# Optimization experiments

Measured on AMD Instinct MI355X. Metric: run time of the kernel, lower is better.

Reference implementation:

```python
import jax, jax.numpy as jnp
import numpy as np

S, NL = 64, 5000          # num_sequences, num_labels
PD, LD = 1024, 768        # protein / label embedding dims
DIM, OD = 512, 512        # latent_dim, output_dim


def setup_inputs() -> dict:
    key = jax.random.key(0)
    ks = jax.random.split(key, 8)
    sc = lambda f: 1.0 / np.sqrt(f).astype(np.float32)
    return {
        "P_f": jax.random.normal(ks[0], (S, PD), jnp.float32),
        "label_emb": jax.random.normal(ks[1], (NL, LD), jnp.float32),
        "W_p": jax.random.normal(ks[2], (DIM, PD), jnp.float32) * sc(PD),
        "W_l": jax.random.normal(ks[3], (DIM, LD), jnp.float32) * sc(LD),
        "W1": jax.random.normal(ks[4], (OD, 2 * DIM), jnp.float32) * sc(2 * DIM),
        "b1": jnp.zeros((OD,), jnp.float32),
        "W2": jax.random.normal(ks[5], (OD, OD), jnp.float32) * sc(OD),
        "b2": jnp.zeros((OD,), jnp.float32),
        "W3": jax.random.normal(ks[6], (1, OD), jnp.float32) * sc(OD),
        "b3": jnp.zeros((1,), jnp.float32),
        "L": jnp.arange(NL, dtype=jnp.int64),
    }


def reference(P_f, label_emb, W_p, W_l, W1, b1, W2, b2, W3, b3, L):
    # label lookup (cached_label_embeddings(L)) + linear projections
    L_f = label_emb[L]                      # [NL, LD]
    P_e = P_f @ W_p.T                       # [S, DIM]
    L_e = L_f @ W_l.T                       # [NL, DIM]
    # joint cat([P_e_expanded, L_e_expanded]) @ W1.T  ==  P-side + L-side GEMMs,
    # broadcast-summed (avoids materializing the [S*NL, 2*DIM] concat)
    hp = P_e @ W1[:, :DIM].T                # [S, OD]
    hl = L_e @ W1[:, DIM:].T                # [NL, OD]
    h = jax.nn.relu(hp[:, None, :] + hl[None, :, :] + b1)   # [S, NL, OD]
    h = jax.nn.relu(jnp.einsum("snd,od->sno", h, W2) + b2)  # [S, NL, OD]
    logits = jnp.einsum("sno,o->sn", h, W3[0]) + b3[0]      # [S, NL]
    return logits
```

## Files before the change

kernel.cpp:

```cpp
#include <hip/hip_runtime.h>
#include <hip/hip_bf16.h>

typedef short short8 __attribute__((ext_vector_type(8)));
typedef float f32x4 __attribute__((ext_vector_type(4)));

#define S_   64
#define NL_  5000
#define PD_  1024
#define LD_  768
#define DIM_ 512
#define OD_  512

#define BK     32
#define NWIN4  4
#define KSTEPS 16
#define NT_M   79
#define HL_RT  157

__device__ __forceinline__ ushort f2bf(float f) {
    union { float f; unsigned u; } v; v.f = f;
    unsigned r = v.u + 0x7fffu + ((v.u >> 16) & 1u);
    return (ushort)(r >> 16);
}
__device__ __forceinline__ float bf2f(ushort h) {
    union { unsigned u; float f; } v; v.u = ((unsigned)h) << 16;
    return v.f;
}
__device__ __forceinline__ int swz(int row, int kslot) {
    return (row * 64 + kslot * 16) ^ (((row >> 1) & 7) << 4);
}

__device__ __forceinline__ void proj8(
    float* Af , const float* __restrict__ A, int lda, int K,
    const float* __restrict__ W, int ldw, const float* __restrict__ bias,
    float* __restrict__ C, int o0, int t) {
    const int s = t & 63, og = t >> 6;
    const int oA = o0 + og * 2, oB = oA + 1;
    float acc0 = 0.f, acc1 = 0.f;
    for (int ck = 0; ck < K; ck += 256) {
        __syncthreads();
#pragma unroll
        for (int it = 0; it < 16; it++) {
            int r = it * 4 + (t >> 6);
            float4 v = *(const float4*)(A + (size_t)r * lda + ck + (t & 63) * 4);
            *(float4*)(Af + r * 258 + (t & 63) * 4) = v;
        }
        __syncthreads();
        const float* w0 = W + (size_t)oA * ldw + ck;
        const float* w1 = W + (size_t)oB * ldw + ck;
        const float* ar = Af + s * 258;
#pragma unroll 8
        for (int k4 = 0; k4 < 64; k4++) {
            f32x4 a4 = *(const f32x4*)(ar + k4 * 4);
            float4 v0 = *(const float4*)(w0 + k4 * 4);
            float4 v1 = *(const float4*)(w1 + k4 * 4);
            acc0 += a4[0] * v0.x + a4[1] * v0.y + a4[2] * v0.z + a4[3] * v0.w;
            acc1 += a4[0] * v1.x + a4[1] * v1.y + a4[2] * v1.z + a4[3] * v1.w;
        }
    }
    C[s * DIM_ + oA] = acc0 + (bias ? bias[oA] : 0.f);
    C[s * DIM_ + oB] = acc1 + (bias ? bias[oB] : 0.f);
}

__global__ __launch_bounds__(256) void k_pre1(
    const float* __restrict__ W2, const float* __restrict__ W_l,
    const float* __restrict__ W1, const float* __restrict__ P_f,
    const float* __restrict__ W_p,
    char* __restrict__ panel, ushort* __restrict__ MlT, float* __restrict__ P_e) {
    __shared__ float lbuf[64 * 258];
    int b = blockIdx.x, t = threadIdx.x;
    if (b < 128) {
        int c = b * 256 + t;
        int o = c >> 6, rem = c & 63, kt = rem >> 2, kslot = rem & 3;
        const float* src = W2 + o * DIM_ + kt * BK + kslot * 8;
        float4 v0 = *(const float4*)src;
        float4 v1 = *(const float4*)(src + 4);
        union { ushort u[8]; short8 v; } pk;
        pk.u[0] = f2bf(v0.x); pk.u[1] = f2bf(v0.y); pk.u[2] = f2bf(v0.z); pk.u[3] = f2bf(v0.w);
        pk.u[4] = f2bf(v1.x); pk.u[5] = f2bf(v1.y); pk.u[6] = f2bf(v1.z); pk.u[7] = f2bf(v1.w);
        *(short8*)(panel + kt * 32768 + (o >> 4) * 1024 + kslot * 256 + (o & 15) * 16) = pk.v;
    } else if (b < 320) {
        float (*w1r)[DIM_] = (float (*)[DIM_])lbuf;
        int bx = b - 128;
        int o0 = (bx / 3) * 8;
        int ld = (bx % 3) * 256 + t;
        for (int i = t; i < 8 * DIM_; i += 256)
            w1r[i >> 9][i & 511] = W1[(o0 + (i >> 9)) * (2 * DIM_) + DIM_ + (i & 511)];
        __syncthreads();
        float acc[8] = {};
        for (int dim = 0; dim < DIM_; dim += 4) {
            float wl0 = W_l[(dim + 0) * LD_ + ld];
            float wl1 = W_l[(dim + 1) * LD_ + ld];
            float wl2 = W_l[(dim + 2) * LD_ + ld];
            float wl3 = W_l[(dim + 3) * LD_ + ld];
#pragma unroll
            for (int oi = 0; oi < 8; oi++) {
                f32x4 wv = *(const f32x4*)&w1r[oi][dim];
                acc[oi] += wv[0] * wl0 + wv[1] * wl1 + wv[2] * wl2 + wv[3] * wl3;
            }
        }
#pragma unroll
        for (int oi = 0; oi < 8; oi++) MlT[(o0 + oi) * LD_ + ld] = f2bf(acc[oi]);
    } else {
        proj8(lbuf, P_f, PD_, PD_, W_p, PD_, nullptr, P_e, (b - 320) * 8, t);
    }
}

__global__ __launch_bounds__(256) void k_pre2(
    const float* __restrict__ P_e, const float* __restrict__ W1,
    const float* __restrict__ b1, const float* __restrict__ emb,
    const int* __restrict__ L, const ushort* __restrict__ MlT,
    float* __restrict__ hpb, ushort* __restrict__ hlB) {
    __shared__ float lbuf[64 * 258];
    int b = blockIdx.x, t = threadIdx.x;
    if (b < 64) {
        proj8(lbuf, P_e, DIM_, DIM_, W1, 2 * DIM_, b1, hpb, b * 8, t);
    } else {
        int hb = b - 64;
        int rblk = hb % HL_RT, oh = hb / HL_RT;
        int r0 = rblk * 32;
        int w = t >> 6, l = t & 63, lg = l >> 4, ll = l & 15;
        const float* arow[2];
#pragma unroll
        for (int mt = 0; mt < 2; mt++) {
            int r = r0 + mt * 16 + ll;
            if (r >= NL_) r = NL_ - 1;
            arow[mt] = emb + (size_t)L[r] * LD_ + lg * 8;
        }
        f32x4 acc[2][4] = {};
        for (int k = 0; k < LD_; k += 32) {
            short8 a[2], bf[4];
#pragma unroll
            for (int mt = 0; mt < 2; mt++) {
                float4 v0 = *(const float4*)(arow[mt] + k);
                float4 v1 = *(const float4*)(arow[mt] + k + 4);
                union { ushort u[8]; short8 v; } pk;
                pk.u[0] = f2bf(v0.x); pk.u[1] = f2bf(v0.y);
                pk.u[2] = f2bf(v0.z); pk.u[3] = f2bf(v0.w);
                pk.u[4] = f2bf(v1.x); pk.u[5] = f2bf(v1.y);
                pk.u[6] = f2bf(v1.z); pk.u[7] = f2bf(v1.w);
                a[mt] = pk.v;
            }
#pragma unroll
            for (int ot = 0; ot < 4; ot++) {
                int o = oh * 256 + w * 64 + ot * 16 + ll;
                bf[ot] = *(const short8*)(MlT + o * LD_ + k + lg * 8);
            }
#pragma unroll
            for (int mt = 0; mt < 2; mt++)
#pragma unroll
                for (int ot = 0; ot < 4; ot++)
                    acc[mt][ot] = __builtin_amdgcn_mfma_f32_16x16x32_bf16(a[mt], bf[ot], acc[mt][ot], 0, 0, 0);
        }
#pragma unroll
        for (int mt = 0; mt < 2; mt++)
#pragma unroll
            for (int ot = 0; ot < 4; ot++)
#pragma unroll
                for (int reg = 0; reg < 4; reg++) {
                    int r = r0 + mt * 16 + lg * 4 + reg;
                    if (r < NL_)
                        hlB[(size_t)r * DIM_ + oh * 256 + w * 64 + ot * 16 + ll] = f2bf(acc[mt][ot][reg]);
                }
    }
}

__global__ __launch_bounds__(512, 2) void k_main2(
    const ushort* __restrict__ hlB, const float* __restrict__ hpb,
    const char* __restrict__ panel, const float* __restrict__ b2,
    const float* __restrict__ W3, const float* __restrict__ b3,
    float* __restrict__ out) {
    __shared__ f32x4 ldsv[4096];
    char* lds = (char*)ldsv;
    const int t = threadIdx.x;
    const int n0 = blockIdx.x * 64, s0 = blockIdx.y * 2;
    const int w = t >> 6, lane = t & 63, lg = lane >> 4, ll = lane & 15;
    const int wr = w >> 2, wc = w & 3;

    const int arow = t >> 2, akslot = t & 3;
    int an = n0 + (arow & 63); if (an >= NL_) an = NL_ - 1;
    const ushort* hlsrc = hlB + (size_t)an * DIM_ + akslot * 8;
    const float*  hpsrc = hpb + (s0 + (arow >> 6)) * DIM_ + akslot * 8;
    const int awz = swz(arow, akslot);

    const int abase = swz(wr * 64 + ll, lg);
    const char* bbase = panel + (wc * 8) * 1024 + lane * 16;

    f32x4 acc[4][8] = {};

    auto packSub = [&](int buf, int sub, short8 hv, f32x4 p0, f32x4 p1) {
        float x[8];
#pragma unroll
        for (int e = 0; e < 4; e++) {
            float a0 = bf2f((ushort)hv[e]) + p0[e];
            float a1 = bf2f((ushort)hv[4 + e]) + p1[e];
            x[e]     = a0 > 0.f ? a0 : 0.f;
            x[4 + e] = a1 > 0.f ? a1 : 0.f;
        }
        union { __hip_bfloat162 h2[4]; short8 v; } pk;
#pragma unroll
        for (int e = 0; e < 4; e++)
            pk.h2[e] = __float22bfloat162_rn(make_float2(x[2 * e], x[2 * e + 1]));
        *(short8*)(lds + buf * 32768 + sub * 8192 + awz) = pk.v;
    };

    {
#pragma unroll
        for (int i = 0; i < 4; i++) {
            short8 hv = *(const short8*)(hlsrc + i * BK);
            f32x4 p0 = *(const f32x4*)(hpsrc + i * BK);
            f32x4 p1 = *(const f32x4*)(hpsrc + i * BK + 4);
            packSub(0, i, hv, p0, p1);
        }
        asm volatile("s_waitcnt lgkmcnt(0)" ::: "memory");
        __builtin_amdgcn_s_barrier();
    }
    short8 bq0[4], bq1[4];
#pragma unroll
    for (int j = 0; j < 4; j++) bq0[j] = *(const short8*)(bbase + j * 1024);

    short8 hvA, hvB; f32x4 pA0, pA1, pB0, pB1;

    for (int win = 0; win < NWIN4; win++) {
        const char* A = lds + (win & 1) * 32768;
        const int nxt = (win & 1) ^ 1;
        const bool more = (win + 1 < NWIN4);
#pragma unroll
        for (int i = 0; i < 4; i++) {
            const int ks = 4 * win + i;
            const char* bks = bbase + ks * 32768;
            short8 a[4];
#pragma unroll
            for (int mt = 0; mt < 4; mt++)
                a[mt] = *(const short8*)(A + i * 8192 + abase + mt * 1024);
#pragma unroll
            for (int j = 0; j < 4; j++) bq1[j] = *(const short8*)(bks + 4096 + j * 1024);
            if (more) {
                if (i == 0) {
                    hvA = *(const short8*)(hlsrc + (ks + 4) * BK);
                    pA0 = *(const f32x4*)(hpsrc + (ks + 4) * BK);
                    pA1 = *(const f32x4*)(hpsrc + (ks + 4) * BK + 4);
                } else if (i == 1) {
                    packSub(nxt, 0, hvA, pA0, pA1);
                    hvB = *(const short8*)(hlsrc + (ks + 4) * BK);
                    pB0 = *(const f32x4*)(hpsrc + (ks + 4) * BK);
                    pB1 = *(const f32x4*)(hpsrc + (ks + 4) * BK + 4);
                } else if (i == 2) {
                    packSub(nxt, 1, hvB, pB0, pB1);
                    hvA = *(const short8*)(hlsrc + (ks + 4) * BK);
                    pA0 = *(const f32x4*)(hpsrc + (ks + 4) * BK);
                    pA1 = *(const f32x4*)(hpsrc + (ks + 4) * BK + 4);
                } else {
                    packSub(nxt, 2, hvA, pA0, pA1);
                    hvB = *(const short8*)(hlsrc + (ks + 4) * BK);
                    pB0 = *(const f32x4*)(hpsrc + (ks + 4) * BK);
                    pB1 = *(const f32x4*)(hpsrc + (ks + 4) * BK + 4);
                }
            }
            __builtin_amdgcn_s_setprio(1);
#pragma unroll
            for (int mt = 0; mt < 4; mt++)
#pragma unroll
                for (int j = 0; j < 4; j++)
                    acc[mt][j] = __builtin_amdgcn_mfma_f32_16x16x32_bf16(a[mt], bq0[j], acc[mt][j], 0, 0, 0);
            __builtin_amdgcn_s_setprio(0);
            if (!(win == NWIN4 - 1 && i == 3))
#pragma unroll
                for (int j = 0; j < 4; j++)
                    bq0[j] = *(const short8*)(bbase + (ks + 1) * 32768 + j * 1024);
            __builtin_amdgcn_s_setprio(1);
#pragma unroll
            for (int mt = 0; mt < 4; mt++)
#pragma unroll
                for (int j = 0; j < 4; j++)
                    acc[mt][4 + j] = __builtin_amdgcn_mfma_f32_16x16x32_bf16(a[mt], bq1[j], acc[mt][4 + j], 0, 0, 0);
            __builtin_amdgcn_s_setprio(0);
        }
        if (more) packSub(nxt, 3, hvB, pB0, pB1);
        asm volatile("s_waitcnt lgkmcnt(0)" ::: "memory");
        __builtin_amdgcn_s_barrier();
    }

    float* logit = (float*)lds;
    if (t < 128) logit[t] = 0.f;
    __syncthreads();
#pragma unroll
    for (int mt = 0; mt < 4; mt++) {
        float p4[4] = { 0.f, 0.f, 0.f, 0.f };
#pragma unroll
        for (int ot = 0; ot < 8; ot++) {
            int o = wc * 128 + ot * 16 + ll;
            float bb = b2[o], w3 = W3[o];
#pragma unroll
            for (int reg = 0; reg < 4; reg++) {
                float v = acc[mt][ot][reg] + bb;
                v = v > 0.f ? v : 0.f;
                p4[reg] += v * w3;
            }
        }
#pragma unroll
        for (int m = 1; m < 16; m <<= 1)
#pragma unroll
            for (int reg = 0; reg < 4; reg++) p4[reg] += __shfl_xor(p4[reg], m, 64);
        if (ll == 0)
#pragma unroll
            for (int reg = 0; reg < 4; reg++)
                atomicAdd(&logit[wr * 64 + mt * 16 + lg * 4 + reg], p4[reg]);
    }
    __syncthreads();
    if (t < 128) {
        int n = n0 + (t & 63);
        int s = s0 + (t >> 6);
        if (n < NL_) out[(size_t)s * NL_ + n] = logit[t] + b3[0];
    }
}

extern "C" void kernel_launch(void* const* d_in, const int* in_sizes, int n_in,
                              void* d_out, int out_size, void* d_ws, size_t ws_size,
                              hipStream_t stream) {
    const float* P_f = (const float*)d_in[0];
    const float* emb = (const float*)d_in[1];
    const float* W_p = (const float*)d_in[2];
    const float* W_l = (const float*)d_in[3];
    const float* W1  = (const float*)d_in[4];
    const float* b1  = (const float*)d_in[5];
    const float* W2  = (const float*)d_in[6];
    const float* b2  = (const float*)d_in[7];
    const float* W3  = (const float*)d_in[8];
    const float* b3  = (const float*)d_in[9];
    const int*   L   = (const int*)d_in[10];
    float* out = (float*)d_out;

    char* ws = (char*)d_ws;
    size_t off = 0;
    auto alloc = [&](size_t bytes) {
        void* p = ws + off;
        off = (off + bytes + 255) & ~(size_t)255;
        return p;
    };
    char*   panel = (char*)alloc((size_t)KSTEPS * 32768);
    ushort* MlT   = (ushort*)alloc((size_t)OD_ * LD_ * 2);
    float*  P_e   = (float*)alloc((size_t)S_ * DIM_ * 4);
    float*  hpb   = (float*)alloc((size_t)S_ * DIM_ * 4);
    ushort* hlB   = (ushort*)alloc((size_t)NL_ * DIM_ * 2);

    k_pre1<<<384, 256, 0, stream>>>(W2, W_l, W1, P_f, W_p, panel, MlT, P_e);
    k_pre2<<<378, 256, 0, stream>>>(P_e, W1, b1, emb, L, MlT, hpb, hlB);
    k_main2<<<dim3(NT_M, 32), 512, 0, stream>>>(hlB, hpb, panel, b2, W3, b3, out);
}
```

Measured before the change: 241.5 us.

## Stage full A tile in LDS upfront and drop windowed double-buffering

The main MLP kernel now builds the entire 128x512 relu(hl+hp) bf16 A tile into a 128KB LDS buffer before the GEMM loop, replacing the 4-window double-buffered pipeline that interleaved global loads and packing with MFMA work. The K loop becomes a simple 16-step loop with no per-window barriers or in-loop packing. This removes barrier and scheduling overhead inside the loop, but exposes all global load latency in a prologue and doubles LDS use, which can cut occupancy below the two blocks per CU requested by launch bounds.

```diff
diff --git a/kernel.cpp b/kernel.cpp
--- a/kernel.cpp
+++ b/kernel.cpp
@@ -12,7 +12,6 @@
 #define OD_  512
 
 #define BK     32
-#define NWIN4  4
 #define KSTEPS 16
 #define NT_M   79
 #define HL_RT  157
@@ -170,7 +169,7 @@
     const char* __restrict__ panel, const float* __restrict__ b2,
     const float* __restrict__ W3, const float* __restrict__ b3,
     float* __restrict__ out) {
-    __shared__ f32x4 ldsv[4096];
+    __shared__ f32x4 ldsv[8192];
     char* lds = (char*)ldsv;
     const int t = threadIdx.x;
     const int n0 = blockIdx.x * 64, s0 = blockIdx.y * 2;
@@ -188,7 +187,7 @@
 
     f32x4 acc[4][8] = {};
 
-    auto packSub = [&](int buf, int sub, short8 hv, f32x4 p0, f32x4 p1) {
+    auto packSub = [&](int sub, short8 hv, f32x4 p0, f32x4 p1) {
         float x[8];
 #pragma unroll
         for (int e = 0; e < 4; e++) {
@@ -201,86 +200,60 @@
 #pragma unroll
         for (int e = 0; e < 4; e++)
             pk.h2[e] = __float22bfloat162_rn(make_float2(x[2 * e], x[2 * e + 1]));
-        *(short8*)(lds + buf * 32768 + sub * 8192 + awz) = pk.v;
+        *(short8*)(lds + sub * 8192 + awz) = pk.v;
     };
 
-    {
+#pragma unroll
+    for (int g = 0; g < 4; g++) {
+        short8 hv[4]; f32x4 p0[4], p1[4];
 #pragma unroll
         for (int i = 0; i < 4; i++) {
-            short8 hv = *(const short8*)(hlsrc + i * BK);
-            f32x4 p0 = *(const f32x4*)(hpsrc + i * BK);
-            f32x4 p1 = *(const f32x4*)(hpsrc + i * BK + 4);
-            packSub(0, i, hv, p0, p1);
-        }
-        asm volatile("s_waitcnt lgkmcnt(0)" ::: "memory");
-        __builtin_amdgcn_s_barrier();
-    }
+            int ks = g * 4 + i;
+            hv[i] = *(const short8*)(hlsrc + ks * BK);
+            p0[i] = *(const f32x4*)(hpsrc + ks * BK);
+            p1[i] = *(const f32x4*)(hpsrc + ks * BK + 4);
+        }
+#pragma unroll
+        for (int i = 0; i < 4; i++) packSub(g * 4 + i, hv[i], p0[i], p1[i]);
+        __builtin_amdgcn_sched_barrier(0);
+    }
+    asm volatile("s_waitcnt lgkmcnt(0)" ::: "memory");
+    __builtin_amdgcn_s_barrier();
+
     short8 bq0[4], bq1[4];
 #pragma unroll
     for (int j = 0; j < 4; j++) bq0[j] = *(const short8*)(bbase + j * 1024);
 
-    short8 hvA, hvB; f32x4 pA0, pA1, pB0, pB1;
-
-    for (int win = 0; win < NWIN4; win++) {
-        const char* A = lds + (win & 1) * 32768;
-        const int nxt = (win & 1) ^ 1;
-        const bool more = (win + 1 < NWIN4);
-#pragma unroll
-        for (int i = 0; i < 4; i++) {
-            const int ks = 4 * win + i;
-            const char* bks = bbase + ks * 32768;
-            short8 a[4];
-#pragma unroll
-            for (int mt = 0; mt < 4; mt++)
-                a[mt] = *(const short8*)(A + i * 8192 + abase + mt * 1024);
-#pragma unroll
-            for (int j = 0; j < 4; j++) bq1[j] = *(const short8*)(bks + 4096 + j * 1024);
-            if (more) {
-                if (i == 0) {
-                    hvA = *(const short8*)(hlsrc + (ks + 4) * BK);
-                    pA0 = *(const f32x4*)(hpsrc + (ks + 4) * BK);
-                    pA1 = *(const f32x4*)(hpsrc + (ks + 4) * BK + 4);
-                } else if (i == 1) {
-                    packSub(nxt, 0, hvA, pA0, pA1);
-                    hvB = *(const short8*)(hlsrc + (ks + 4) * BK);
-                    pB0 = *(const f32x4*)(hpsrc + (ks + 4) * BK);
-                    pB1 = *(const f32x4*)(hpsrc + (ks + 4) * BK + 4);
-                } else if (i == 2) {
-                    packSub(nxt, 1, hvB, pB0, pB1);
-                    hvA = *(const short8*)(hlsrc + (ks + 4) * BK);
-                    pA0 = *(const f32x4*)(hpsrc + (ks + 4) * BK);
-                    pA1 = *(const f32x4*)(hpsrc + (ks + 4) * BK + 4);
-                } else {
-                    packSub(nxt, 2, hvA, pA0, pA1);
-                    hvB = *(const short8*)(hlsrc + (ks + 4) * BK);
-                    pB0 = *(const f32x4*)(hpsrc + (ks + 4) * BK);
-                    pB1 = *(const f32x4*)(hpsrc + (ks + 4) * BK + 4);
-                }
-            }
-            __builtin_amdgcn_s_setprio(1);
-#pragma unroll
-            for (int mt = 0; mt < 4; mt++)
-#pragma unroll
-                for (int j = 0; j < 4; j++)
-                    acc[mt][j] = __builtin_amdgcn_mfma_f32_16x16x32_bf16(a[mt], bq0[j], acc[mt][j], 0, 0, 0);
-            __builtin_amdgcn_s_setprio(0);
-            if (!(win == NWIN4 - 1 && i == 3))
-#pragma unroll
-                for (int j = 0; j < 4; j++)
-                    bq0[j] = *(const short8*)(bbase + (ks + 1) * 32768 + j * 1024);
-            __builtin_amdgcn_s_setprio(1);
-#pragma unroll
-            for (int mt = 0; mt < 4; mt++)
-#pragma unroll
-                for (int j = 0; j < 4; j++)
-                    acc[mt][4 + j] = __builtin_amdgcn_mfma_f32_16x16x32_bf16(a[mt], bq1[j], acc[mt][4 + j], 0, 0, 0);
-            __builtin_amdgcn_s_setprio(0);
-        }
-        if (more) packSub(nxt, 3, hvB, pB0, pB1);
-        asm volatile("s_waitcnt lgkmcnt(0)" ::: "memory");
-        __builtin_amdgcn_s_barrier();
-    }
-
+    for (int ks = 0; ks < KSTEPS; ks++) {
+        const char* A = lds + ks * 8192;
+        const char* bks = bbase + ks * 32768;
+        short8 a[4];
+#pragma unroll
+        for (int mt = 0; mt < 4; mt++)
+            a[mt] = *(const short8*)(A + abase + mt * 1024);
+#pragma unroll
+        for (int j = 0; j < 4; j++) bq1[j] = *(const short8*)(bks + 4096 + j * 1024);
+        __builtin_amdgcn_s_setprio(1);
+#pragma unroll
+        for (int mt = 0; mt < 4; mt++)
+#pragma unroll
+            for (int j = 0; j < 4; j++)
+                acc[mt][j] = __builtin_amdgcn_mfma_f32_16x16x32_bf16(a[mt], bq0[j], acc[mt][j], 0, 0, 0);
+        __builtin_amdgcn_s_setprio(0);
+        if (ks + 1 < KSTEPS)
+#pragma unroll
+            for (int j = 0; j < 4; j++)
+                bq0[j] = *(const short8*)(bks + 32768 + j * 1024);
+        __builtin_amdgcn_s_setprio(1);
+#pragma unroll
+        for (int mt = 0; mt < 4; mt++)
+#pragma unroll
+            for (int j = 0; j < 4; j++)
+                acc[mt][4 + j] = __builtin_amdgcn_mfma_f32_16x16x32_bf16(a[mt], bq1[j], acc[mt][4 + j], 0, 0, 0);
+        __builtin_amdgcn_s_setprio(0);
+    }
+
+    __syncthreads();
     float* logit = (float*)lds;
     if (t < 128) logit[t] = 0.f;
     __syncthreads();
```

After: 238.9 us, median of 2. Within noise of the previous version (-1.1%).

## Retile main kernel to 4 sequences per block and split output dim across blocks

Applied to the files above, without the earlier changes.

The main fused MLP kernel now handles 4 sequences per block instead of 2, so each hl tile load is reused for twice as many sequences. The output dimension is split across two blocks in a z grid dimension, with the warp layout changed from 2x4 to 4x2. Partial logits go to a workspace buffer, and a new combine kernel sums the two halves and adds b3. LDS use doubles to 128KB per block, which may limit occupancy below the launch bound of 2, and the extra launch plus partial-buffer traffic add cost.

```diff
diff --git a/kernel.cpp b/kernel.cpp
--- a/kernel.cpp
+++ b/kernel.cpp
@@ -168,61 +168,82 @@
 __global__ __launch_bounds__(512, 2) void k_main2(
     const ushort* __restrict__ hlB, const float* __restrict__ hpb,
     const char* __restrict__ panel, const float* __restrict__ b2,
-    const float* __restrict__ W3, const float* __restrict__ b3,
-    float* __restrict__ out) {
-    __shared__ f32x4 ldsv[4096];
+    const float* __restrict__ W3, float* __restrict__ part) {
+    __shared__ f32x4 ldsv[8192];
     char* lds = (char*)ldsv;
     const int t = threadIdx.x;
-    const int n0 = blockIdx.x * 64, s0 = blockIdx.y * 2;
+    const int n0 = blockIdx.x * 64, s0 = blockIdx.y * 4, oh = blockIdx.z;
     const int w = t >> 6, lane = t & 63, lg = lane >> 4, ll = lane & 15;
-    const int wr = w >> 2, wc = w & 3;
+    const int wr = w >> 1, wc = w & 1;
 
     const int arow = t >> 2, akslot = t & 3;
     int an = n0 + (arow & 63); if (an >= NL_) an = NL_ - 1;
     const ushort* hlsrc = hlB + (size_t)an * DIM_ + akslot * 8;
-    const float*  hpsrc = hpb + (s0 + (arow >> 6)) * DIM_ + akslot * 8;
+    const float*  hpA = hpb + (s0 + (t >> 8)) * DIM_ + akslot * 8;
+    const float*  hpB = hpA + 2 * DIM_;
     const int awz = swz(arow, akslot);
 
     const int abase = swz(wr * 64 + ll, lg);
-    const char* bbase = panel + (wc * 8) * 1024 + lane * 16;
+    const char* bbase = panel + (oh * 16 + wc * 8) * 1024 + lane * 16;
 
     f32x4 acc[4][8] = {};
 
-    auto packSub = [&](int buf, int sub, short8 hv, f32x4 p0, f32x4 p1) {
+    auto packCore = [&](int buf, int sub, short8 hv,
+                        f32x4 a0, f32x4 a1, f32x4 b0, f32x4 b1) {
+        union { __hip_bfloat162 h2[4]; short8 v; } pk;
         float x[8];
 #pragma unroll
         for (int e = 0; e < 4; e++) {
-            float a0 = bf2f((ushort)hv[e]) + p0[e];
-            float a1 = bf2f((ushort)hv[4 + e]) + p1[e];
-            x[e]     = a0 > 0.f ? a0 : 0.f;
-            x[4 + e] = a1 > 0.f ? a1 : 0.f;
-        }
-        union { __hip_bfloat162 h2[4]; short8 v; } pk;
+            float u0 = bf2f((ushort)hv[e]) + a0[e];
+            float u1 = bf2f((ushort)hv[4 + e]) + a1[e];
+            x[e] = u0 > 0.f ? u0 : 0.f;
+            x[4 + e] = u1 > 0.f ? u1 : 0.f;
+        }
 #pragma unroll
         for (int e = 0; e < 4; e++)
             pk.h2[e] = __float22bfloat162_rn(make_float2(x[2 * e], x[2 * e + 1]));
-        *(short8*)(lds + buf * 32768 + sub * 8192 + awz) = pk.v;
+        *(short8*)(lds + buf * 65536 + sub * 16384 + awz) = pk.v;
+#pragma unroll
+        for (int e = 0; e < 4; e++) {
+            float u0 = bf2f((ushort)hv[e]) + b0[e];
+            float u1 = bf2f((ushort)hv[4 + e]) + b1[e];
+            x[e] = u0 > 0.f ? u0 : 0.f;
+            x[4 + e] = u1 > 0.f ? u1 : 0.f;
+        }
+#pragma unroll
+        for (int e = 0; e < 4; e++)
+            pk.h2[e] = __float22bfloat162_rn(make_float2(x[2 * e], x[2 * e + 1]));
+        *(short8*)(lds + buf * 65536 + sub * 16384 + 8192 + awz) = pk.v;
     };
-
-    {
-#pragma unroll
-        for (int i = 0; i < 4; i++) {
-            short8 hv = *(const short8*)(hlsrc + i * BK);
-            f32x4 p0 = *(const f32x4*)(hpsrc + i * BK);
-            f32x4 p1 = *(const f32x4*)(hpsrc + i * BK + 4);
-            packSub(0, i, hv, p0, p1);
-        }
-        asm volatile("s_waitcnt lgkmcnt(0)" ::: "memory");
-        __builtin_amdgcn_s_barrier();
-    }
+    auto packLazy = [&](int buf, int sub, short8 hv, int ks) {
+        f32x4 a0 = *(const f32x4*)(hpA + ks * BK);
+        f32x4 a1 = *(const f32x4*)(hpA + ks * BK + 4);
+        f32x4 b0 = *(const f32x4*)(hpB + ks * BK);
+        f32x4 b1 = *(const f32x4*)(hpB + ks * BK + 4);
+        packCore(buf, sub, hv, a0, a1, b0, b1);
+    };
+
+#pragma unroll
+    for (int g = 0; g < 2; g++) {
+#pragma unroll
+        for (int i = 0; i < 2; i++) {
+            int ks = g * 2 + i;
+            short8 hv = *(const short8*)(hlsrc + ks * BK);
+            packLazy(0, ks, hv, ks);
+        }
+        __builtin_amdgcn_sched_barrier(0);
+    }
+    asm volatile("s_waitcnt lgkmcnt(0)" ::: "memory");
+    __builtin_amdgcn_s_barrier();
+
     short8 bq0[4], bq1[4];
 #pragma unroll
     for (int j = 0; j < 4; j++) bq0[j] = *(const short8*)(bbase + j * 1024);
 
-    short8 hvA, hvB; f32x4 pA0, pA1, pB0, pB1;
+    short8 hvA, hvB; f32x4 pB0a, pB1a, pB0b, pB1b;
 
     for (int win = 0; win < NWIN4; win++) {
-        const char* A = lds + (win & 1) * 32768;
+        const char* A = lds + (win & 1) * 65536;
         const int nxt = (win & 1) ^ 1;
         const bool more = (win + 1 < NWIN4);
 #pragma unroll
@@ -232,29 +253,29 @@
             short8 a[4];
 #pragma unroll
             for (int mt = 0; mt < 4; mt++)
-                a[mt] = *(const short8*)(A + i * 8192 + abase + mt * 1024);
+                a[mt] = *(const short8*)(A + i * 16384 + abase + mt * 1024);
 #pragma unroll
             for (int j = 0; j < 4; j++) bq1[j] = *(const short8*)(bks + 4096 + j * 1024);
             if (more) {
                 if (i == 0) {
                     hvA = *(const short8*)(hlsrc + (ks + 4) * BK);
-                    pA0 = *(const f32x4*)(hpsrc + (ks + 4) * BK);
-                    pA1 = *(const f32x4*)(hpsrc + (ks + 4) * BK + 4);
                 } else if (i == 1) {
-                    packSub(nxt, 0, hvA, pA0, pA1);
+                    packLazy(nxt, 0, hvA, ks + 3);
                     hvB = *(const short8*)(hlsrc + (ks + 4) * BK);
-                    pB0 = *(const f32x4*)(hpsrc + (ks + 4) * BK);
-                    pB1 = *(const f32x4*)(hpsrc + (ks + 4) * BK + 4);
+                    pB0a = *(const f32x4*)(hpA + (ks + 4) * BK);
+                    pB1a = *(const f32x4*)(hpA + (ks + 4) * BK + 4);
+                    pB0b = *(const f32x4*)(hpB + (ks + 4) * BK);
+                    pB1b = *(const f32x4*)(hpB + (ks + 4) * BK + 4);
                 } else if (i == 2) {
-                    packSub(nxt, 1, hvB, pB0, pB1);
+                    packCore(nxt, 1, hvB, pB0a, pB1a, pB0b, pB1b);
                     hvA = *(const short8*)(hlsrc + (ks + 4) * BK);
-                    pA0 = *(const f32x4*)(hpsrc + (ks + 4) * BK);
-                    pA1 = *(const f32x4*)(hpsrc + (ks + 4) * BK + 4);
                 } else {
-                    packSub(nxt, 2, hvA, pA0, pA1);
+                    packLazy(nxt, 2, hvA, ks + 3);
                     hvB = *(const short8*)(hlsrc + (ks + 4) * BK);
-                    pB0 = *(const f32x4*)(hpsrc + (ks + 4) * BK);
-                    pB1 = *(const f32x4*)(hpsrc + (ks + 4) * BK + 4);
+                    pB0a = *(const f32x4*)(hpA + (ks + 4) * BK);
+                    pB1a = *(const f32x4*)(hpA + (ks + 4) * BK + 4);
+                    pB0b = *(const f32x4*)(hpB + (ks + 4) * BK);
+                    pB1b = *(const f32x4*)(hpB + (ks + 4) * BK + 4);
                 }
             }
             __builtin_amdgcn_s_setprio(1);
@@ -276,20 +297,20 @@
                     acc[mt][4 + j] = __builtin_amdgcn_mfma_f32_16x16x32_bf16(a[mt], bq1[j], acc[mt][4 + j], 0, 0, 0);
             __builtin_amdgcn_s_setprio(0);
         }
-        if (more) packSub(nxt, 3, hvB, pB0, pB1);
+        if (more) packCore(nxt, 3, hvB, pB0a, pB1a, pB0b, pB1b);
         asm volatile("s_waitcnt lgkmcnt(0)" ::: "memory");
         __builtin_amdgcn_s_barrier();
     }
 
     float* logit = (float*)lds;
-    if (t < 128) logit[t] = 0.f;
+    if (t < 256) logit[t] = 0.f;
     __syncthreads();
 #pragma unroll
     for (int mt = 0; mt < 4; mt++) {
         float p4[4] = { 0.f, 0.f, 0.f, 0.f };
 #pragma unroll
         for (int ot = 0; ot < 8; ot++) {
-            int o = wc * 128 + ot * 16 + ll;
+            int o = oh * 256 + wc * 128 + ot * 16 + ll;
             float bb = b2[o], w3 = W3[o];
 #pragma unroll
             for (int reg = 0; reg < 4; reg++) {
@@ -308,11 +329,18 @@
                 atomicAdd(&logit[wr * 64 + mt * 16 + lg * 4 + reg], p4[reg]);
     }
     __syncthreads();
-    if (t < 128) {
+    if (t < 256) {
         int n = n0 + (t & 63);
         int s = s0 + (t >> 6);
-        if (n < NL_) out[(size_t)s * NL_ + n] = logit[t] + b3[0];
-    }
+        if (n < NL_)
+            part[(size_t)oh * (S_ * NL_) + (size_t)s * NL_ + n] = logit[t];
+    }
+}
+
+__global__ void k_comb(const float* __restrict__ part, const float* __restrict__ b3,
+                       float* __restrict__ out) {
+    int i = blockIdx.x * 256 + threadIdx.x;
+    if (i < S_ * NL_) out[i] = part[i] + part[S_ * NL_ + i] + b3[0];
 }
 
 extern "C" void kernel_launch(void* const* d_in, const int* in_sizes, int n_in,
@@ -343,8 +371,10 @@
     float*  P_e   = (float*)alloc((size_t)S_ * DIM_ * 4);
     float*  hpb   = (float*)alloc((size_t)S_ * DIM_ * 4);
     ushort* hlB   = (ushort*)alloc((size_t)NL_ * DIM_ * 2);
+    float*  part  = (float*)alloc((size_t)2 * S_ * NL_ * 4);
 
     k_pre1<<<384, 256, 0, stream>>>(W2, W_l, W1, P_f, W_p, panel, MlT, P_e);
     k_pre2<<<378, 256, 0, stream>>>(P_e, W1, b1, emb, L, MlT, hpb, hlB);
-    k_main2<<<dim3(NT_M, 32), 512, 0, stream>>>(hlB, hpb, panel, b2, W3, b3, out);
-}
+    k_main2<<<dim3(NT_M, 16, 2), 512, 0, stream>>>(hlB, hpb, panel, b2, W3, part);
+    k_comb<<<(S_ * NL_ + 255) / 256, 256, 0, stream>>>(part, b3, out);
+}
```

Result: slower. 268.1 us (+11.0%).
